# Optimization experiments

Hardware: AMD Instinct MI355X
Metric: run time of the kernel (lower is better)

## Reference

```python
import jax, jax.numpy as jnp
import numpy as np

B, S, D, H, E = 8, 196, 768, 12, 8
HD = D // H  # 64
FF = 4 * D   # 3072
EPS = 1e-5


def setup_inputs() -> dict:
    key = jax.random.key(0)
    ks = jax.random.split(key, 12)
    s = 0.02
    inp = {
        'x': jax.random.normal(ks[0], (B, S, D), jnp.float32),
        'ln1_g': jnp.ones((D,), jnp.float32),
        'ln1_b': jnp.zeros((D,), jnp.float32),
        'Wq': jax.random.normal(ks[1], (D, D), jnp.float32) * s,
        'bq': jnp.zeros((D,), jnp.float32),
        'Wk': jax.random.normal(ks[2], (D, HD), jnp.float32) * s,
        'bk': jnp.zeros((HD,), jnp.float32),
        'Wv': jax.random.normal(ks[3], (D, HD), jnp.float32) * s,
        'bv': jnp.zeros((HD,), jnp.float32),
        'ln2_g': jnp.ones((D,), jnp.float32),
        'ln2_b': jnp.zeros((D,), jnp.float32),
        'Wg': jax.random.normal(ks[4], (D, E), jnp.float32) * s,
        'bg': jnp.zeros((E,), jnp.float32),
        'W1': jax.random.normal(ks[5], (E, D, FF), jnp.float32) * s,
        'b1': jnp.zeros((E, FF), jnp.float32),
        'W2': jax.random.normal(ks[6], (E, FF, D), jnp.float32) * s,
        'b2': jnp.zeros((E, D), jnp.float32),
    }
    return inp


def _layernorm(x, g, b):
    mu = jnp.mean(x, axis=-1, keepdims=True)
    var = jnp.var(x, axis=-1, keepdims=True)
    return (x - mu) * jax.lax.rsqrt(var + EPS) * g + b


def _rotate_half(x):
    x1, x2 = jnp.split(x, 2, axis=-1)
    return jnp.concatenate((-x2, x1), axis=-1)


def _rope(seq_len):
    inv_freq = 1.0 / (10000.0 ** (jnp.arange(0, HD, 2, dtype=jnp.float32) / HD))
    freqs = jnp.arange(seq_len, dtype=jnp.float32)[:, None] * inv_freq[None, :]
    emb = jnp.concatenate((freqs, freqs), axis=-1)  # [S, HD]
    return emb[None, :, None, :]  # [1, S, 1, HD]


def _attention(x, Wq, bq, Wk, bk, Wv, bv):
    b, s, _ = x.shape
    q = (x @ Wq + bq).reshape(b, s, H, HD)
    k = (x @ Wk + bk).reshape(b, s, 1, HD)
    v = (x @ Wv + bv).reshape(b, s, 1, HD)
    k = jnp.broadcast_to(k, (b, s, H, HD))
    v = jnp.broadcast_to(v, (b, s, H, HD))
    pe = _rope(s)
    cos, sin = jnp.cos(pe), jnp.sin(pe)
    q = q * cos + _rotate_half(q) * sin
    k = k * cos + _rotate_half(k) * sin
    scale = HD ** -0.5
    # NOTE: faithful to source -- matmul over the last two dims of [b,s,h,d],
    # i.e. attention across HEADS, not sequence positions.
    attn = jnp.einsum('bshd,bsgd->bshg', q, k) * scale
    attn = jax.nn.softmax(attn, axis=-1)
    out = jnp.einsum('bshg,bsgd->bshd', attn, v)
    return out.reshape(b, s, H * HD)


def _moe(x, Wg, bg, W1, b1, W2, b2):
    b, s, d = x.shape
    xt = x.reshape(-1, d)  # [T, D]
    gates = jax.nn.softmax(xt @ Wg + bg, axis=-1)
    top1 = jnp.argmax(gates, axis=-1)  # topk(k=2)[:,0] == argmax
    out = jnp.zeros_like(xt)
    for e in range(E):  # small fixed expert count
        h = jax.nn.gelu(xt @ W1[e] + b1[e], approximate=False)
        y = h @ W2[e] + b2[e]
        out = jnp.where((top1 == e)[:, None], y, out)
    return out.reshape(b, s, d)


def reference(x, ln1_g, ln1_b, Wq, bq, Wk, bk, Wv, bv, ln2_g, ln2_b, Wg, bg, W1, b1, W2, b2):
    res = x
    h = _layernorm(x, ln1_g, ln1_b)
    h = _attention(h, Wq, bq, Wk, bk, Wv, bv)
    x = res + h
    res = x
    h = _layernorm(x, ln2_g, ln2_b)
    h = _moe(h, Wg, bg, W1, b1, W2, b2)
    return res + h
```

## Files before the change

kernel.cpp:

```cpp
#include <hip/hip_runtime.h>
#include <hip/hip_bf16.h>


typedef unsigned short u16;
typedef short bf16x8_t __attribute__((ext_vector_type(8)));
typedef float f32x4_t  __attribute__((ext_vector_type(4)));

#define T_TOK 1568
#define DM 768
#define HD 64
#define FF 3072
#define NE 8

#define OFF_CNT   0
#define OFF_BUCK  256
#define OFF_H2    (OFF_BUCK + NE*T_TOK*4)
#define OFF_HMID  (OFF_H2 + T_TOK*DM*2)

__device__ __forceinline__ u16 f2bf(float f) {
    return __builtin_bit_cast(u16, __float2bfloat16(f));
}
__device__ __forceinline__ float gelu_f(float x) {
    return 0.5f * x * (1.0f + erff(x * 0.70710678118654752440f));
}

#define SFENCE() __builtin_amdgcn_sched_barrier(0)
#define RAW_BAR() __builtin_amdgcn_s_barrier()

__global__ __launch_bounds__(256) void k_front(
        const float* __restrict__ x,
        const float* __restrict__ g1, const float* __restrict__ b1,
        const float* __restrict__ Wv, const float* __restrict__ bv,
        const float* __restrict__ g2, const float* __restrict__ b2g,
        const float* __restrict__ Wg, const float* __restrict__ bg,
        const float* __restrict__ b2moe,
        u16* __restrict__ h2, float* __restrict__ out,
        int* __restrict__ cnt, int* __restrict__ buck) {
    __shared__ float h1s[8 * DM];
    __shared__ float ps[4 * 8 * 64];
    __shared__ float wgs[NE * DM];
    __shared__ float g2s[DM], b2s[DM];
    int tid = threadIdx.x, tb = blockIdx.x * 8;
    int lane = tid & 63, w = tid >> 6;

    for (int idx = tid; idx < NE * DM; idx += 256) {
        int e = idx / DM, c = idx % DM;
        wgs[idx] = Wg[(size_t)c * NE + e];
    }
    for (int idx = tid; idx < DM; idx += 256) { g2s[idx] = g2[idx]; b2s[idx] = b2g[idx]; }

    float xa[2][12];
#pragma unroll
    for (int ttl = 0; ttl < 2; ttl++) {
        int t = tb + w * 2 + ttl;
        const float* xp = x + (size_t)t * DM;
        float s = 0.0f;
#pragma unroll
        for (int i = 0; i < 12; i++) { float q = xp[lane + 64 * i]; xa[ttl][i] = q; s += q; }
#pragma unroll
        for (int m = 1; m < 64; m <<= 1) s += __shfl_xor(s, m);
        float mu = s * (1.0f / DM);
        float vs = 0.0f;
#pragma unroll
        for (int i = 0; i < 12; i++) { float d = xa[ttl][i] - mu; vs += d * d; }
#pragma unroll
        for (int m = 1; m < 64; m <<= 1) vs += __shfl_xor(vs, m);
        float rs = rsqrtf(vs * (1.0f / DM) + 1e-5f);
        float* hp = h1s + (size_t)(w * 2 + ttl) * DM;
#pragma unroll
        for (int i = 0; i < 12; i++) {
            int c = lane + 64 * i;
            hp[c] = (xa[ttl][i] - mu) * rs * g1[c] + b1[c];
        }
    }
    __syncthreads();

    {
        float acc[8];
#pragma unroll
        for (int tt = 0; tt < 8; tt++) acc[tt] = 0.0f;
        const float* wp = Wv + (size_t)(w * 192) * HD + lane;
#pragma unroll 2
        for (int kk = 0; kk < 192; kk += 4) {
            float w0 = wp[(size_t)(kk + 0) * HD];
            float w1 = wp[(size_t)(kk + 1) * HD];
            float w2 = wp[(size_t)(kk + 2) * HD];
            float w3 = wp[(size_t)(kk + 3) * HD];
            int kb = w * 192 + kk;
#pragma unroll
            for (int tt = 0; tt < 8; tt++) {
                f32x4_t hv = *(const f32x4_t*)&h1s[tt * DM + kb];
                acc[tt] += hv[0] * w0 + hv[1] * w1 + hv[2] * w2 + hv[3] * w3;
            }
        }
#pragma unroll
        for (int tt = 0; tt < 8; tt++) ps[(w * 8 + tt) * 64 + lane] = acc[tt];
    }
    __syncthreads();
    float vred[2];
#pragma unroll
    for (int s2 = 0; s2 < 2; s2++) {
        int tt = w * 2 + s2;
        vred[s2] = ps[tt * 64 + lane] + ps[(8 + tt) * 64 + lane] +
                   ps[(16 + tt) * 64 + lane] + ps[(24 + tt) * 64 + lane] + bv[lane];
    }

#pragma unroll
    for (int ttl = 0; ttl < 2; ttl++) {
        int t = tb + w * 2 + ttl;
        float vl = vred[ttl];
        float xv[12];
        float s = 0.0f;
#pragma unroll
        for (int i = 0; i < 12; i++) { float q = xa[ttl][i] + vl; xv[i] = q; s += q; }
#pragma unroll
        for (int m = 1; m < 64; m <<= 1) s += __shfl_xor(s, m);
        float mu = s * (1.0f / DM);
        float vs = 0.0f;
#pragma unroll
        for (int i = 0; i < 12; i++) { float d = xv[i] - mu; vs += d * d; }
#pragma unroll
        for (int m = 1; m < 64; m <<= 1) vs += __shfl_xor(vs, m);
        float rs = rsqrtf(vs * (1.0f / DM) + 1e-5f);
        float le[NE];
#pragma unroll
        for (int e = 0; e < NE; e++) le[e] = 0.0f;
        u16* h2p = h2 + (size_t)t * DM;
#pragma unroll
        for (int i = 0; i < 12; i++) {
            int c = lane + 64 * i;
            float h = (xv[i] - mu) * rs * g2s[c] + b2s[c];
            h2p[c] = f2bf(h);
#pragma unroll
            for (int e = 0; e < NE; e++) le[e] += h * wgs[e * DM + c];
        }
#pragma unroll
        for (int e = 0; e < NE; e++) {
#pragma unroll
            for (int m = 1; m < 64; m <<= 1) le[e] += __shfl_xor(le[e], m);
        }
        float best = le[0] + bg[0]; int be = 0;
#pragma unroll
        for (int e = 1; e < NE; e++) {
            float q = le[e] + bg[e];
            if (q > best) { best = q; be = e; }
        }
        if (lane == 0) {
            int pos = atomicAdd(&cnt[be], 1);
            buck[be * T_TOK + pos] = t;
        }
        float* op = out + (size_t)t * DM;
        const float* bp = b2moe + (size_t)be * DM;
#pragma unroll
        for (int i = 0; i < 12; i++) {
            int c = lane + 64 * i;
            op[c] = xv[i] + bp[c];
        }
    }
}

__global__ __launch_bounds__(256, 3) void k_moe_gemm1(
        const u16* __restrict__ h2, const float* __restrict__ W1,
        const float* __restrict__ b1, const int* __restrict__ cnt,
        const int* __restrict__ buck, u16* __restrict__ hmid) {
    int nt = blockIdx.x, e = blockIdx.y, mt = blockIdx.z;
    int cnte = cnt[e];
    int m0 = mt * 128;
    if (m0 >= cnte) return;
    int n0 = nt * 64;
    const float* W1e = W1 + (size_t)e * DM * FF;
    __shared__ __align__(16) u16 As[128 * 72];
    __shared__ __align__(16) u16 Bs[64 * 72];
    int tid = threadIdx.x, lane = tid & 63, wid = tid >> 6;

    int arow = tid >> 3, ac = tid & 7;
    int atok[4];
#pragma unroll
    for (int j = 0; j < 4; j++) {
        int i = m0 + arow + 32 * j;
        if (i >= cnte) i = cnte - 1;
        atok[j] = buck[e * T_TOK + i];
    }
    int bn = tid & 63, bkg = tid >> 6;

    f32x4_t acc[2][4];
#pragma unroll
    for (int mi = 0; mi < 2; mi++)
#pragma unroll
        for (int ni = 0; ni < 4; ni++) acc[mi][ni] = (f32x4_t){0.f, 0.f, 0.f, 0.f};

    bf16x8_t aP[4], aQ[4];
    float bP[16], bQ[16];

#define G_LOAD(SA, SB, KT) { \
    int k0_ = (KT) * 64; \
    _Pragma("unroll") \
    for (int j = 0; j < 4; j++) \
        SA[j] = *(const bf16x8_t*)&h2[(size_t)atok[j] * DM + k0_ + ac * 8]; \
    const float* bp_ = W1e + (size_t)(k0_ + bkg * 16) * FF + n0 + bn; \
    _Pragma("unroll") \
    for (int kk = 0; kk < 16; kk++) SB[kk] = bp_[(size_t)kk * FF]; \
}
#define STORE_LDS(SA, SB) { \
    _Pragma("unroll") \
    for (int j = 0; j < 4; j++) \
        *(bf16x8_t*)&As[(arow + 32 * j) * 72 + ac * 8] = SA[j]; \
    bf16x8_t p0_, p1_; \
    _Pragma("unroll") \
    for (int kk = 0; kk < 8; kk++) { \
        p0_[kk] = (short)f2bf(SB[kk]); \
        p1_[kk] = (short)f2bf(SB[kk + 8]); \
    } \
    *(bf16x8_t*)&Bs[bn * 72 + bkg * 16] = p0_; \
    *(bf16x8_t*)&Bs[bn * 72 + bkg * 16 + 8] = p1_; \
}
#define MFMA_TILE() { \
    int lr_ = lane & 15, q_ = lane >> 4; \
    _Pragma("unroll") \
    for (int s = 0; s < 2; s++) { \
        bf16x8_t af[2], bfr[4]; \
        _Pragma("unroll") \
        for (int mi = 0; mi < 2; mi++) \
            af[mi] = *(const bf16x8_t*)&As[(wid * 32 + mi * 16 + lr_) * 72 + s * 32 + q_ * 8]; \
        _Pragma("unroll") \
        for (int ni = 0; ni < 4; ni++) \
            bfr[ni] = *(const bf16x8_t*)&Bs[(ni * 16 + lr_) * 72 + s * 32 + q_ * 8]; \
        _Pragma("unroll") \
        for (int mi = 0; mi < 2; mi++) \
            _Pragma("unroll") \
            for (int ni = 0; ni < 4; ni++) \
                acc[mi][ni] = __builtin_amdgcn_mfma_f32_16x16x32_bf16( \
                    af[mi], bfr[ni], acc[mi][ni], 0, 0, 0); \
    } \
}
#define PHASE(SA, SB, PKT) { \
    SFENCE(); RAW_BAR(); SFENCE(); \
    STORE_LDS(SA, SB) \
    asm volatile("s_waitcnt lgkmcnt(0)" ::: "memory"); \
    SFENCE(); RAW_BAR(); SFENCE(); \
    if ((PKT) < 12) G_LOAD(SA, SB, PKT) \
    MFMA_TILE() \
}

    G_LOAD(aP, bP, 0)
    G_LOAD(aQ, bQ, 1)
    for (int kt = 0; kt < 12; kt += 2) {
        PHASE(aP, bP, kt + 2)
        PHASE(aQ, bQ, kt + 3)
    }
#undef G_LOAD
#undef STORE_LDS
#undef MFMA_TILE
#undef PHASE

    int lr = lane & 15, q = lane >> 4;
    float bias[4];
#pragma unroll
    for (int ni = 0; ni < 4; ni++) bias[ni] = b1[(size_t)e * FF + n0 + ni * 16 + lr];
#pragma unroll
    for (int mi = 0; mi < 2; mi++) {
#pragma unroll
        for (int r = 0; r < 4; r++) {
            int i = m0 + wid * 32 + mi * 16 + q * 4 + r;
            if (i < cnte) {
                int t = buck[e * T_TOK + i];
                size_t base = (size_t)t * FF + n0;
#pragma unroll
                for (int ni = 0; ni < 4; ni++) {
                    float vv = acc[mi][ni][r] + bias[ni];
                    hmid[base + ni * 16 + lr] = f2bf(gelu_f(vv));
                }
            }
        }
    }
}

__global__ __launch_bounds__(256, 3) void k_moe_gemm2(
        const u16* __restrict__ hmid, const float* __restrict__ W2,
        const int* __restrict__ cnt, const int* __restrict__ buck,
        float* __restrict__ out) {
    int nt = blockIdx.x, e = blockIdx.y, z = blockIdx.z;
    int kc = z & 3, mt = z >> 2;
    int cnte = cnt[e];
    int m0 = mt * 128;
    if (m0 >= cnte) return;
    int n0 = nt * 64;
    int kbase = kc * (FF / 4);
    const float* W2e = W2 + (size_t)e * FF * DM;
    __shared__ __align__(16) u16 As[128 * 72];
    __shared__ __align__(16) u16 Bs[64 * 72];
    int tid = threadIdx.x, lane = tid & 63, wid = tid >> 6;

    int arow = tid >> 3, ac = tid & 7;
    int atok[4];
#pragma unroll
    for (int j = 0; j < 4; j++) {
        int i = m0 + arow + 32 * j;
        if (i >= cnte) i = cnte - 1;
        atok[j] = buck[e * T_TOK + i];
    }
    int bn = tid & 63, bkg = tid >> 6;

    f32x4_t acc[2][4];
#pragma unroll
    for (int mi = 0; mi < 2; mi++)
#pragma unroll
        for (int ni = 0; ni < 4; ni++) acc[mi][ni] = (f32x4_t){0.f, 0.f, 0.f, 0.f};

    bf16x8_t aP[4], aQ[4];
    float bP[16], bQ[16];

#define G_LOAD(SA, SB, KT) { \
    int k0_ = kbase + (KT) * 64; \
    _Pragma("unroll") \
    for (int j = 0; j < 4; j++) \
        SA[j] = *(const bf16x8_t*)&hmid[(size_t)atok[j] * FF + k0_ + ac * 8]; \
    const float* bp_ = W2e + (size_t)(k0_ + bkg * 16) * DM + n0 + bn; \
    _Pragma("unroll") \
    for (int kk = 0; kk < 16; kk++) SB[kk] = bp_[(size_t)kk * DM]; \
}
#define STORE_LDS(SA, SB) { \
    _Pragma("unroll") \
    for (int j = 0; j < 4; j++) \
        *(bf16x8_t*)&As[(arow + 32 * j) * 72 + ac * 8] = SA[j]; \
    bf16x8_t p0_, p1_; \
    _Pragma("unroll") \
    for (int kk = 0; kk < 8; kk++) { \
        p0_[kk] = (short)f2bf(SB[kk]); \
        p1_[kk] = (short)f2bf(SB[kk + 8]); \
    } \
    *(bf16x8_t*)&Bs[bn * 72 + bkg * 16] = p0_; \
    *(bf16x8_t*)&Bs[bn * 72 + bkg * 16 + 8] = p1_; \
}
#define MFMA_TILE() { \
    int lr_ = lane & 15, q_ = lane >> 4; \
    _Pragma("unroll") \
    for (int s = 0; s < 2; s++) { \
        bf16x8_t af[2], bfr[4]; \
        _Pragma("unroll") \
        for (int mi = 0; mi < 2; mi++) \
            af[mi] = *(const bf16x8_t*)&As[(wid * 32 + mi * 16 + lr_) * 72 + s * 32 + q_ * 8]; \
        _Pragma("unroll") \
        for (int ni = 0; ni < 4; ni++) \
            bfr[ni] = *(const bf16x8_t*)&Bs[(ni * 16 + lr_) * 72 + s * 32 + q_ * 8]; \
        _Pragma("unroll") \
        for (int mi = 0; mi < 2; mi++) \
            _Pragma("unroll") \
            for (int ni = 0; ni < 4; ni++) \
                acc[mi][ni] = __builtin_amdgcn_mfma_f32_16x16x32_bf16( \
                    af[mi], bfr[ni], acc[mi][ni], 0, 0, 0); \
    } \
}
#define PHASE(SA, SB, PKT) { \
    SFENCE(); RAW_BAR(); SFENCE(); \
    STORE_LDS(SA, SB) \
    asm volatile("s_waitcnt lgkmcnt(0)" ::: "memory"); \
    SFENCE(); RAW_BAR(); SFENCE(); \
    if ((PKT) < 12) G_LOAD(SA, SB, PKT) \
    MFMA_TILE() \
}

    G_LOAD(aP, bP, 0)
    G_LOAD(aQ, bQ, 1)
    for (int kt = 0; kt < 12; kt += 2) {
        PHASE(aP, bP, kt + 2)
        PHASE(aQ, bQ, kt + 3)
    }
#undef G_LOAD
#undef STORE_LDS
#undef MFMA_TILE
#undef PHASE

    int lr = lane & 15, q = lane >> 4;
#pragma unroll
    for (int mi = 0; mi < 2; mi++) {
#pragma unroll
        for (int r = 0; r < 4; r++) {
            int i = m0 + wid * 32 + mi * 16 + q * 4 + r;
            if (i < cnte) {
                int t = buck[e * T_TOK + i];
                size_t base = (size_t)t * DM + n0;
#pragma unroll
                for (int ni = 0; ni < 4; ni++)
                    atomicAdd(&out[base + ni * 16 + lr], acc[mi][ni][r]);
            }
        }
    }
}

extern "C" void kernel_launch(void* const* d_in, const int* in_sizes, int n_in,
                              void* d_out, int out_size, void* d_ws, size_t ws_size,
                              hipStream_t stream) {
    const float* x    = (const float*)d_in[0];
    const float* ln1g = (const float*)d_in[1];
    const float* ln1b = (const float*)d_in[2];
    const float* Wv   = (const float*)d_in[7];
    const float* bv   = (const float*)d_in[8];
    const float* ln2g = (const float*)d_in[9];
    const float* ln2b = (const float*)d_in[10];
    const float* Wg   = (const float*)d_in[11];
    const float* bg   = (const float*)d_in[12];
    const float* W1   = (const float*)d_in[13];
    const float* b1   = (const float*)d_in[14];
    const float* W2   = (const float*)d_in[15];
    const float* b2   = (const float*)d_in[16];

    char* ws = (char*)d_ws;
    int*   cnt  = (int*)(ws + OFF_CNT);
    int*   buck = (int*)(ws + OFF_BUCK);
    u16*   h2   = (u16*)(ws + OFF_H2);
    u16*   hmid = (u16*)(ws + OFF_HMID);
    float* out  = (float*)d_out;

    hipMemsetAsync(cnt, 0, NE * sizeof(int), stream);
    k_front<<<T_TOK / 8, 256, 0, stream>>>(x, ln1g, ln1b, Wv, bv, ln2g, ln2b,
                                           Wg, bg, b2, h2, out, cnt, buck);
    k_moe_gemm1<<<dim3(FF / 64, NE, 13), 256, 0, stream>>>(h2, W1, b1, cnt, buck, hmid);
    k_moe_gemm2<<<dim3(DM / 64, NE, 52), 256, 0, stream>>>(hmid, W2, cnt, buck, out);
}
```

Before: 276.2 us.

## Remap front kernel to one 64-thread block per token with vectorized loads

The fused LayerNorm/V-projection/gating kernel now runs one wavefront per token instead of 8 tokens per 256-thread block. This removes the split-K partial-sum buffer, its extra barrier, and the shared-memory staging of Wg and the LN2 parameters. All row loads and stores become 128-bit, and the bf16 output is written four values at a time. In exchange, each token's block re-reads the full Wv and Wg matrices, raising cache traffic roughly eightfold for the projection weights.

After: 285.5 us. +3.4%, slower.

```diff
diff --git a/kernel.cpp b/kernel.cpp
--- a/kernel.cpp
+++ b/kernel.cpp
@@ -4,6 +4,7 @@
 
 typedef unsigned short u16;
 typedef short bf16x8_t __attribute__((ext_vector_type(8)));
+typedef unsigned short u16x4_t __attribute__((ext_vector_type(4)));
 typedef float f32x4_t  __attribute__((ext_vector_type(4)));
 
 #define T_TOK 1568
@@ -27,7 +28,7 @@
 #define SFENCE() __builtin_amdgcn_sched_barrier(0)
 #define RAW_BAR() __builtin_amdgcn_s_barrier()
 
-__global__ __launch_bounds__(256) void k_front(
+__global__ __launch_bounds__(64) void k_front(
         const float* __restrict__ x,
         const float* __restrict__ g1, const float* __restrict__ b1,
         const float* __restrict__ Wv, const float* __restrict__ bv,
@@ -36,126 +37,128 @@
         const float* __restrict__ b2moe,
         u16* __restrict__ h2, float* __restrict__ out,
         int* __restrict__ cnt, int* __restrict__ buck) {
-    __shared__ float h1s[8 * DM];
-    __shared__ float ps[4 * 8 * 64];
-    __shared__ float wgs[NE * DM];
-    __shared__ float g2s[DM], b2s[DM];
-    int tid = threadIdx.x, tb = blockIdx.x * 8;
-    int lane = tid & 63, w = tid >> 6;
-
-    for (int idx = tid; idx < NE * DM; idx += 256) {
-        int e = idx / DM, c = idx % DM;
-        wgs[idx] = Wg[(size_t)c * NE + e];
-    }
-    for (int idx = tid; idx < DM; idx += 256) { g2s[idx] = g2[idx]; b2s[idx] = b2g[idx]; }
-
-    float xa[2][12];
-#pragma unroll
-    for (int ttl = 0; ttl < 2; ttl++) {
-        int t = tb + w * 2 + ttl;
-        const float* xp = x + (size_t)t * DM;
-        float s = 0.0f;
-#pragma unroll
-        for (int i = 0; i < 12; i++) { float q = xp[lane + 64 * i]; xa[ttl][i] = q; s += q; }
-#pragma unroll
-        for (int m = 1; m < 64; m <<= 1) s += __shfl_xor(s, m);
-        float mu = s * (1.0f / DM);
-        float vs = 0.0f;
-#pragma unroll
-        for (int i = 0; i < 12; i++) { float d = xa[ttl][i] - mu; vs += d * d; }
-#pragma unroll
-        for (int m = 1; m < 64; m <<= 1) vs += __shfl_xor(vs, m);
-        float rs = rsqrtf(vs * (1.0f / DM) + 1e-5f);
-        float* hp = h1s + (size_t)(w * 2 + ttl) * DM;
-#pragma unroll
-        for (int i = 0; i < 12; i++) {
-            int c = lane + 64 * i;
-            hp[c] = (xa[ttl][i] - mu) * rs * g1[c] + b1[c];
+    __shared__ __align__(16) float h1s[DM];
+    __shared__ __align__(16) float vsh[HD];
+    int t = blockIdx.x;
+    int lane = threadIdx.x;
+
+    const float* xp = x + (size_t)t * DM;
+    f32x4_t xv[3];
+    float s = 0.0f;
+#pragma unroll
+    for (int i = 0; i < 3; i++) {
+        xv[i] = *(const f32x4_t*)&xp[4 * lane + 256 * i];
+        s += xv[i][0] + xv[i][1] + xv[i][2] + xv[i][3];
+    }
+#pragma unroll
+    for (int m = 1; m < 64; m <<= 1) s += __shfl_xor(s, m);
+    float mu = s * (1.0f / DM);
+    float vs = 0.0f;
+#pragma unroll
+    for (int i = 0; i < 3; i++)
+#pragma unroll
+        for (int m = 0; m < 4; m++) { float d = xv[i][m] - mu; vs += d * d; }
+#pragma unroll
+    for (int m = 1; m < 64; m <<= 1) vs += __shfl_xor(vs, m);
+    float rs = rsqrtf(vs * (1.0f / DM) + 1e-5f);
+#pragma unroll
+    for (int i = 0; i < 3; i++) {
+        int c = 4 * lane + 256 * i;
+        f32x4_t gg = *(const f32x4_t*)&g1[c];
+        f32x4_t bb = *(const f32x4_t*)&b1[c];
+        f32x4_t h;
+#pragma unroll
+        for (int m = 0; m < 4; m++) h[m] = (xv[i][m] - mu) * rs * gg[m] + bb[m];
+        *(f32x4_t*)&h1s[c] = h;
+    }
+    __syncthreads();
+
+    {
+        float a0 = 0.f, a1 = 0.f, a2 = 0.f, a3 = 0.f;
+        const float* wp = Wv + lane;
+#pragma unroll 2
+        for (int k = 0; k < DM; k += 8) {
+            f32x4_t h0 = *(const f32x4_t*)&h1s[k];
+            f32x4_t h4 = *(const f32x4_t*)&h1s[k + 4];
+            a0 += h0[0] * wp[(size_t)(k + 0) * HD] + h4[0] * wp[(size_t)(k + 4) * HD];
+            a1 += h0[1] * wp[(size_t)(k + 1) * HD] + h4[1] * wp[(size_t)(k + 5) * HD];
+            a2 += h0[2] * wp[(size_t)(k + 2) * HD] + h4[2] * wp[(size_t)(k + 6) * HD];
+            a3 += h0[3] * wp[(size_t)(k + 3) * HD] + h4[3] * wp[(size_t)(k + 7) * HD];
         }
+        vsh[lane] = a0 + a1 + a2 + a3 + bv[lane];
     }
     __syncthreads();
 
-    {
-        float acc[8];
-#pragma unroll
-        for (int tt = 0; tt < 8; tt++) acc[tt] = 0.0f;
-        const float* wp = Wv + (size_t)(w * 192) * HD + lane;
-#pragma unroll 2
-        for (int kk = 0; kk < 192; kk += 4) {
-            float w0 = wp[(size_t)(kk + 0) * HD];
-            float w1 = wp[(size_t)(kk + 1) * HD];
-            float w2 = wp[(size_t)(kk + 2) * HD];
-            float w3 = wp[(size_t)(kk + 3) * HD];
-            int kb = w * 192 + kk;
-#pragma unroll
-            for (int tt = 0; tt < 8; tt++) {
-                f32x4_t hv = *(const f32x4_t*)&h1s[tt * DM + kb];
-                acc[tt] += hv[0] * w0 + hv[1] * w1 + hv[2] * w2 + hv[3] * w3;
-            }
+    f32x4_t vv = *(const f32x4_t*)&vsh[4 * (lane & 15)];
+    float s2 = 0.0f;
+#pragma unroll
+    for (int i = 0; i < 3; i++)
+#pragma unroll
+        for (int m = 0; m < 4; m++) { xv[i][m] += vv[m]; s2 += xv[i][m]; }
+#pragma unroll
+    for (int m = 1; m < 64; m <<= 1) s2 += __shfl_xor(s2, m);
+    float mu2 = s2 * (1.0f / DM);
+    float vs2 = 0.0f;
+#pragma unroll
+    for (int i = 0; i < 3; i++)
+#pragma unroll
+        for (int m = 0; m < 4; m++) { float d = xv[i][m] - mu2; vs2 += d * d; }
+#pragma unroll
+    for (int m = 1; m < 64; m <<= 1) vs2 += __shfl_xor(vs2, m);
+    float rs2 = rsqrtf(vs2 * (1.0f / DM) + 1e-5f);
+
+    float le[NE];
+#pragma unroll
+    for (int e = 0; e < NE; e++) le[e] = 0.0f;
+    u16* h2p = h2 + (size_t)t * DM;
+#pragma unroll
+    for (int i = 0; i < 3; i++) {
+        int c = 4 * lane + 256 * i;
+        f32x4_t gg = *(const f32x4_t*)&g2[c];
+        f32x4_t bb = *(const f32x4_t*)&b2g[c];
+        float h[4];
+        u16x4_t hb;
+#pragma unroll
+        for (int m = 0; m < 4; m++) {
+            h[m] = (xv[i][m] - mu2) * rs2 * gg[m] + bb[m];
+            hb[m] = f2bf(h[m]);
         }
-#pragma unroll
-        for (int tt = 0; tt < 8; tt++) ps[(w * 8 + tt) * 64 + lane] = acc[tt];
-    }
-    __syncthreads();
-    float vred[2];
-#pragma unroll
-    for (int s2 = 0; s2 < 2; s2++) {
-        int tt = w * 2 + s2;
-        vred[s2] = ps[tt * 64 + lane] + ps[(8 + tt) * 64 + lane] +
-                   ps[(16 + tt) * 64 + lane] + ps[(24 + tt) * 64 + lane] + bv[lane];
-    }
-
-#pragma unroll
-    for (int ttl = 0; ttl < 2; ttl++) {
-        int t = tb + w * 2 + ttl;
-        float vl = vred[ttl];
-        float xv[12];
-        float s = 0.0f;
-#pragma unroll
-        for (int i = 0; i < 12; i++) { float q = xa[ttl][i] + vl; xv[i] = q; s += q; }
-#pragma unroll
-        for (int m = 1; m < 64; m <<= 1) s += __shfl_xor(s, m);
-        float mu = s * (1.0f / DM);
-        float vs = 0.0f;
-#pragma unroll
-        for (int i = 0; i < 12; i++) { float d = xv[i] - mu; vs += d * d; }
-#pragma unroll
-        for (int m = 1; m < 64; m <<= 1) vs += __shfl_xor(vs, m);
-        float rs = rsqrtf(vs * (1.0f / DM) + 1e-5f);
-        float le[NE];
-#pragma unroll
-        for (int e = 0; e < NE; e++) le[e] = 0.0f;
-        u16* h2p = h2 + (size_t)t * DM;
-#pragma unroll
-        for (int i = 0; i < 12; i++) {
-            int c = lane + 64 * i;
-            float h = (xv[i] - mu) * rs * g2s[c] + b2s[c];
-            h2p[c] = f2bf(h);
-#pragma unroll
-            for (int e = 0; e < NE; e++) le[e] += h * wgs[e * DM + c];
+        *(u16x4_t*)&h2p[c] = hb;
+#pragma unroll
+        for (int m = 0; m < 4; m++) {
+            f32x4_t w0 = *(const f32x4_t*)&Wg[(size_t)(c + m) * NE];
+            f32x4_t w1 = *(const f32x4_t*)&Wg[(size_t)(c + m) * NE + 4];
+            le[0] += h[m] * w0[0]; le[1] += h[m] * w0[1];
+            le[2] += h[m] * w0[2]; le[3] += h[m] * w0[3];
+            le[4] += h[m] * w1[0]; le[5] += h[m] * w1[1];
+            le[6] += h[m] * w1[2]; le[7] += h[m] * w1[3];
         }
-#pragma unroll
-        for (int e = 0; e < NE; e++) {
-#pragma unroll
-            for (int m = 1; m < 64; m <<= 1) le[e] += __shfl_xor(le[e], m);
-        }
-        float best = le[0] + bg[0]; int be = 0;
-#pragma unroll
-        for (int e = 1; e < NE; e++) {
-            float q = le[e] + bg[e];
-            if (q > best) { best = q; be = e; }
-        }
-        if (lane == 0) {
-            int pos = atomicAdd(&cnt[be], 1);
-            buck[be * T_TOK + pos] = t;
-        }
-        float* op = out + (size_t)t * DM;
-        const float* bp = b2moe + (size_t)be * DM;
-#pragma unroll
-        for (int i = 0; i < 12; i++) {
-            int c = lane + 64 * i;
-            op[c] = xv[i] + bp[c];
-        }
+    }
+#pragma unroll
+    for (int e = 0; e < NE; e++) {
+#pragma unroll
+        for (int m = 1; m < 64; m <<= 1) le[e] += __shfl_xor(le[e], m);
+    }
+    float best = le[0] + bg[0]; int be = 0;
+#pragma unroll
+    for (int e = 1; e < NE; e++) {
+        float q = le[e] + bg[e];
+        if (q > best) { best = q; be = e; }
+    }
+    if (lane == 0) {
+        int pos = atomicAdd(&cnt[be], 1);
+        buck[be * T_TOK + pos] = t;
+    }
+    float* op = out + (size_t)t * DM;
+    const float* bp = b2moe + (size_t)be * DM;
+#pragma unroll
+    for (int i = 0; i < 3; i++) {
+        int c = 4 * lane + 256 * i;
+        f32x4_t bbv = *(const f32x4_t*)&bp[c];
+        f32x4_t o;
+#pragma unroll
+        for (int m = 0; m < 4; m++) o[m] = xv[i][m] + bbv[m];
+        *(f32x4_t*)&op[c] = o;
     }
 }
 
@@ -413,8 +416,8 @@
     float* out  = (float*)d_out;
 
     hipMemsetAsync(cnt, 0, NE * sizeof(int), stream);
-    k_front<<<T_TOK / 8, 256, 0, stream>>>(x, ln1g, ln1b, Wv, bv, ln2g, ln2b,
-                                           Wg, bg, b2, h2, out, cnt, buck);
+    k_front<<<T_TOK, 64, 0, stream>>>(x, ln1g, ln1b, Wv, bv, ln2g, ln2b,
+                                      Wg, bg, b2, h2, out, cnt, buck);
     k_moe_gemm1<<<dim3(FF / 64, NE, 13), 256, 0, stream>>>(h2, W1, b1, cnt, buck, hmid);
     k_moe_gemm2<<<dim3(DM / 64, NE, 52), 256, 0, stream>>>(hmid, W2, cnt, buck, out);
 }
```
